# Kernel optimization log

Measured on AMD Instinct MI355X. Metric: run time of the kernel, lower is better.

Reference implementation:

```python
import jax, jax.numpy as jnp
import numpy as np

N = 100000   # num nodes
C = 128      # in_channels == out_channels
H = 4        # heads
D = C // H   # per-head dim = 32
E = 200000   # edges per edge type
T = 3        # number of edge types


def setup_inputs() -> dict:
    key = jax.random.key(0)
    ks = jax.random.split(key, 13)
    x = jax.random.normal(ks[0], (N, C), jnp.float32)
    src = jax.random.randint(ks[1], (T, E), 0, N, dtype=jnp.int32)
    dst = jax.random.randint(ks[2], (T, E), 0, N, dtype=jnp.int32)
    w = lambda k, shape: (jax.random.normal(k, shape, jnp.float32) * 0.02)
    # per-edge-type TransformerConv params: query/key/value/skip linears (C -> H*D = C)
    Wq, Wk, Wv, Ws = (w(ks[3], (T, C, C)), w(ks[4], (T, C, C)),
                      w(ks[5], (T, C, C)), w(ks[6], (T, C, C)))
    bq, bk, bv, bs = (w(ks[7], (T, C)), w(ks[8], (T, C)),
                      w(ks[9], (T, C)), w(ks[10], (T, C)))
    # fusion linear: (T*C) -> C
    Wf = w(ks[11], (C, T * C))
    bf = w(ks[12], (C,))
    return dict(x=x, src=src, dst=dst, Wq=Wq, bq=bq, Wk=Wk, bk=bk,
                Wv=Wv, bv=bv, Ws=Ws, bs=bs, Wf=Wf, bf=bf)


def _transformer_conv(x, s, d, Wq, bq, Wk, bk, Wv, bv, Ws, bs):
    # PyG TransformerConv (beta=False, root_weight=True, concat=True, eval mode)
    q = (x @ Wq.T + bq).reshape(N, H, D)
    k = (x @ Wk.T + bk).reshape(N, H, D)
    v = (x @ Wv.T + bv).reshape(N, H, D)
    # per-edge attention logits: [E, H]
    alpha = jnp.einsum('ehd,ehd->eh', q[d], k[s]) / np.float32(np.sqrt(D))
    # segment softmax over incoming edges of each destination node
    amax = jax.ops.segment_max(alpha, d, num_segments=N)           # [N, H]
    ex = jnp.exp(alpha - amax[d])                                  # [E, H]
    denom = jax.ops.segment_sum(ex, d, num_segments=N)             # [N, H]
    attn = ex / (denom[d] + 1e-16)                                 # [E, H]
    out = jax.ops.segment_sum(attn[:, :, None] * v[s], d, num_segments=N)  # [N, H, D]
    return out.reshape(N, C) + (x @ Ws.T + bs)  # root/skip connection


def reference(x, src, dst, Wq, bq, Wk, bk, Wv, bv, Ws, bs, Wf, bf):
    outs = [
        _transformer_conv(x, src[t], dst[t], Wq[t], bq[t], Wk[t], bk[t],
                          Wv[t], bv[t], Ws[t], bs[t])
        for t in range(T)
    ]
    combined = jnp.concatenate(outs, axis=-1)  # [N, T*C]
    return combined @ Wf.T + bf                # [N, C]
```

## Files before the change

### kernel.cpp

```cpp
#include <hip/hip_runtime.h>

#define NN 100000
#define CC 128
#define EE 200000
#define TT 3
#define NCHUNK 98

typedef __attribute__((ext_vector_type(8))) __bf16 bf16x8;
typedef __attribute__((ext_vector_type(8))) unsigned short ushort8;
typedef __attribute__((ext_vector_type(4))) float f32x4;

union U8 { ushort8 u; bf16x8 b; };

__device__ __forceinline__ unsigned short f2bf(float v) {
    unsigned u = __float_as_uint(v);
    u += 0x7fffu + ((u >> 16) & 1u);
    return (unsigned short)(u >> 16);
}
__device__ __forceinline__ float bf2f(unsigned short h) {
    return __uint_as_float(((unsigned)h) << 16);
}
__device__ __forceinline__ void split8(const float* f, bf16x8& hi, bf16x8& lo) {
    U8 h, l;
    #pragma unroll
    for (int j = 0; j < 8; ++j) {
        float v = f[j];
        unsigned short hs = f2bf(v);
        h.u[j] = hs;
        l.u[j] = f2bf(v - bf2f(hs));
    }
    hi = h.b; lo = l.b;
}

__device__ __forceinline__ void loadA(const float* __restrict__ X, int arow, int kt, int kb,
                                      bf16x8& hi, bf16x8& lo) {
    float tmp[8];
    if (arow < NN) {
        const float* xp = X + (size_t)arow * CC + kt * 32 + kb * 8;
        float4 p0 = *(const float4*)xp;
        float4 p1 = *(const float4*)(xp + 4);
        tmp[0] = p0.x; tmp[1] = p0.y; tmp[2] = p0.z; tmp[3] = p0.w;
        tmp[4] = p1.x; tmp[5] = p1.y; tmp[6] = p1.z; tmp[7] = p1.w;
    } else {
        #pragma unroll
        for (int j = 0; j < 8; ++j) tmp[j] = 0.f;
    }
    split8(tmp, hi, lo);
}


__global__ __launch_bounds__(256) void k_pack(
    const float* __restrict__ Wq, const float* __restrict__ bq,
    const float* __restrict__ Wk, const float* __restrict__ bk,
    const float* __restrict__ Wv, const float* __restrict__ bv,
    const float* __restrict__ Wf,
    unsigned short* __restrict__ Whi3, unsigned short* __restrict__ Wlo3,
    unsigned short* __restrict__ Wfhi, unsigned short* __restrict__ Wflo,
    float* __restrict__ Bpack)
{
    int idx = blockIdx.x * 256 + threadIdx.x;
    int y = blockIdx.y;
    int j  = idx & 7;
    int l  = (idx >> 3) & 63;
    int nt = (idx >> 9) & 7;
    int kt = idx >> 12;
    int c = nt * 16 + (l & 15);
    int k = kt * 32 + ((l >> 4) << 3) + j;
    if (y < 9) {
        int t = y / 3, m = y % 3;
        const float* W = (m == 0 ? Wq : m == 1 ? Wk : Wv) + t * CC * CC;
        float v = W[c * CC + k];
        unsigned short hs = f2bf(v);
        Whi3[y * CC * CC + idx] = hs;
        Wlo3[y * CC * CC + idx] = f2bf(v - bf2f(hs));
    } else if (y < 12) {
        int t = y - 9;
        float v = Wf[(size_t)c * (TT * CC) + t * CC + k];
        unsigned short hs = f2bf(v);
        Wfhi[t * CC * CC + idx] = hs;
        Wflo[t * CC * CC + idx] = f2bf(v - bf2f(hs));
    } else {
        if (idx < 9 * CC) {
            int mm = idx >> 7, cc2 = idx & 127;
            int t = mm / 3, m = mm % 3;
            const float* b = (m == 0 ? bq : m == 1 ? bk : bv);
            Bpack[idx] = b[t * CC + cc2];
        }
    }
}

__global__ __launch_bounds__(256) void k_wcomb(
    const float* __restrict__ Ws, const float* __restrict__ bs,
    const float* __restrict__ Wf, const float* __restrict__ bf,
    unsigned short* __restrict__ Wch, unsigned short* __restrict__ Wcl,
    float* __restrict__ bconst)
{
    int b = blockIdx.x;
    if (b < 64) {
        int idx = b * 256 + threadIdx.x;
        int k = idx >> 7, c = idx & 127;
        float s = 0.f;
        for (int t = 0; t < TT; ++t) {
            const float* wsp = Ws + t * CC * CC;
            const float* wfp = Wf + (size_t)c * (TT * CC) + t * CC;
            for (int j = 0; j < CC; ++j)
                s += wsp[j * CC + k] * wfp[j];
        }
        int kt = k >> 5, kb = (k >> 3) & 3, j = k & 7;
        int l = (c & 15) + (kb << 4);
        int nt = c >> 4;
        int o = (((kt * 8 + nt) * 64) + l) * 8 + j;
        unsigned short hs = f2bf(s);
        Wch[o] = hs;
        Wcl[o] = f2bf(s - bf2f(hs));
    } else {
        int c = threadIdx.x;
        if (c < CC) {
            float s = bf[c];
            for (int t = 0; t < TT; ++t) {
                const float* wfp = Wf + (size_t)c * (TT * CC) + t * CC;
                for (int j = 0; j < CC; ++j)
                    s += bs[t * CC + j] * wfp[j];
            }
            bconst[c] = s;
        }
    }
}

__global__ __launch_bounds__(256) void k_count(const int* __restrict__ dst, int* __restrict__ deg) {
    int idx = blockIdx.x * 256 + threadIdx.x;
    if (idx >= TT * EE) return;
    int t = idx / EE;
    atomicAdd(&deg[t * NN + dst[idx]], 1);
}

__global__ __launch_bounds__(256) void k_scan1(const int* __restrict__ deg,
                                               int* __restrict__ incl, int* __restrict__ bsums) {
    int t = blockIdx.y, b = blockIdx.x, tid = threadIdx.x;
    const int* d = deg + t * NN;
    int base = b * 1024 + tid * 4;
    int v0 = (base + 0 < NN) ? d[base + 0] : 0;
    int v1 = (base + 1 < NN) ? d[base + 1] : 0;
    int v2 = (base + 2 < NN) ? d[base + 2] : 0;
    int v3 = (base + 3 < NN) ? d[base + 3] : 0;
    v1 += v0; v2 += v1; v3 += v2;
    __shared__ int lds[256];
    lds[tid] = v3;
    for (int off = 1; off < 256; off <<= 1) {
        __syncthreads();
        int x = (tid >= off) ? lds[tid - off] : 0;
        __syncthreads();
        lds[tid] += x;
    }
    __syncthreads();
    int excl = lds[tid] - v3;
    if (base + 0 < NN) incl[t * NN + base + 0] = excl + v0;
    if (base + 1 < NN) incl[t * NN + base + 1] = excl + v1;
    if (base + 2 < NN) incl[t * NN + base + 2] = excl + v2;
    if (base + 3 < NN) incl[t * NN + base + 3] = excl + v3;
    if (tid == 255) bsums[t * NCHUNK + b] = lds[255];
}

__global__ __launch_bounds__(128) void k_scan2(const int* __restrict__ bsums, int* __restrict__ bexcl) {
    int t = blockIdx.y, tid = threadIdx.x;
    __shared__ int lds[128];
    int v = (tid < NCHUNK) ? bsums[t * NCHUNK + tid] : 0;
    lds[tid] = v;
    for (int off = 1; off < 128; off <<= 1) {
        __syncthreads();
        int x = (tid >= off) ? lds[tid - off] : 0;
        __syncthreads();
        lds[tid] += x;
    }
    if (tid < NCHUNK) bexcl[t * NCHUNK + tid] = lds[tid] - v;
}

__global__ __launch_bounds__(256) void k_scan3(const int* __restrict__ deg, const int* __restrict__ incl,
                                               const int* __restrict__ bexcl,
                                               int* __restrict__ offs, int* __restrict__ cursor) {
    int t = blockIdx.y, b = blockIdx.x, tid = threadIdx.x;
    int add = bexcl[t * NCHUNK + b];
    int base = b * 1024 + tid * 4;
    #pragma unroll
    for (int j = 0; j < 4; j++) {
        int i = base + j;
        if (i < NN) {
            int e = incl[t * NN + i] - deg[t * NN + i] + add;
            offs[t * NN + i] = e;
            cursor[t * NN + i] = e;
        }
    }
}

__global__ __launch_bounds__(256) void k_scatter(const int* __restrict__ src, const int* __restrict__ dst,
                                                 int* __restrict__ cursor, int* __restrict__ csr_src) {
    int idx = blockIdx.x * 256 + threadIdx.x;
    if (idx >= TT * EE) return;
    int t = idx / EE;
    int d = dst[idx];
    int pos = atomicAdd(&cursor[t * NN + d], 1);
    csr_src[t * EE + pos] = src[idx];
}

__global__ __launch_bounds__(256, 2) void k_mg3(
    const float* __restrict__ x,
    const unsigned short* __restrict__ Whi, const unsigned short* __restrict__ Wlo,
    const float* __restrict__ B3,
    float* __restrict__ Q, float* __restrict__ K, float* __restrict__ V)
{
    int wid = threadIdx.x >> 6, l = threadIdx.x & 63;
    int lan = l & 15, kb = l >> 4;
    int rb = blockIdx.x * 128 + wid * 32;

    bf16x8 ah[2][4], al[2][4];
    #pragma unroll
    for (int rt = 0; rt < 2; ++rt)
        #pragma unroll
        for (int kt = 0; kt < 4; ++kt)
            loadA(x, rb + rt * 16 + lan, kt, kb, ah[rt][kt], al[rt][kt]);

    #pragma unroll 1
    for (int m = 0; m < 3; ++m) {
        const unsigned short* wh = Whi + m * CC * CC;
        const unsigned short* wl = Wlo + m * CC * CC;
        f32x4 acc[2][8];
        #pragma unroll
        for (int rt = 0; rt < 2; ++rt)
            #pragma unroll
            for (int nt = 0; nt < 8; ++nt)
                #pragma unroll
                for (int i = 0; i < 4; ++i) acc[rt][nt][i] = 0.f;

        #pragma unroll
        for (int kt = 0; kt < 4; ++kt) {
            #pragma unroll
            for (int nc = 0; nc < 2; ++nc) {
                U8 bh[4], bl[4];
                #pragma unroll
                for (int j = 0; j < 4; ++j) {
                    size_t wo = ((size_t)(kt * 8 + nc * 4 + j) * 64 + l) * 8;
                    bh[j].u = *(const ushort8*)(wh + wo);
                    bl[j].u = *(const ushort8*)(wl + wo);
                }
                #pragma unroll
                for (int j = 0; j < 4; ++j) {
                    int nt = nc * 4 + j;
                    #pragma unroll
                    for (int rt = 0; rt < 2; ++rt) {
                        acc[rt][nt] = __builtin_amdgcn_mfma_f32_16x16x32_bf16(ah[rt][kt], bl[j].b, acc[rt][nt], 0, 0, 0);
                        acc[rt][nt] = __builtin_amdgcn_mfma_f32_16x16x32_bf16(al[rt][kt], bh[j].b, acc[rt][nt], 0, 0, 0);
                        acc[rt][nt] = __builtin_amdgcn_mfma_f32_16x16x32_bf16(ah[rt][kt], bh[j].b, acc[rt][nt], 0, 0, 0);
                    }
                }
            }
        }

        float* dst = (m == 0 ? Q : m == 1 ? K : V);
        #pragma unroll
        for (int nt = 0; nt < 8; ++nt) {
            int col = nt * 16 + lan;
            float bias = B3[m * CC + col];
            #pragma unroll
            for (int rt = 0; rt < 2; ++rt)
                #pragma unroll
                for (int i = 0; i < 4; ++i) {
                    int grow = rb + rt * 16 + kb * 4 + i;
                    if (grow < NN)
                        dst[(size_t)grow * CC + col] = acc[rt][nt][i] + bias;
                }
        }
    }
}

__global__ __launch_bounds__(256, 2) void k_mfuse(
    const float* __restrict__ X0,
    const unsigned short* __restrict__ W0h, const unsigned short* __restrict__ W0l,
    const float* __restrict__ X1,
    const unsigned short* __restrict__ W1h, const unsigned short* __restrict__ W1l,
    const float* __restrict__ bias, float* __restrict__ out, int accum)
{
    int wid = threadIdx.x >> 6, l = threadIdx.x & 63;
    int lan = l & 15, kb = l >> 4;
    int rb = blockIdx.x * 128 + wid * 32;

    f32x4 acc[2][8];
    #pragma unroll
    for (int rt = 0; rt < 2; ++rt)
        #pragma unroll
        for (int nt = 0; nt < 8; ++nt)
            #pragma unroll
            for (int i = 0; i < 4; ++i) acc[rt][nt][i] = 0.f;

    #pragma unroll 1
    for (int s = 0; s < 2; ++s) {
        const float* X = s ? X1 : X0;
        if (!X) break;
        const unsigned short* wh = s ? W1h : W0h;
        const unsigned short* wl = s ? W1l : W0l;

        bf16x8 ah[2][4], al[2][4];
        #pragma unroll
        for (int rt = 0; rt < 2; ++rt)
            #pragma unroll
            for (int kt = 0; kt < 4; ++kt)
                loadA(X, rb + rt * 16 + lan, kt, kb, ah[rt][kt], al[rt][kt]);

        #pragma unroll
        for (int kt = 0; kt < 4; ++kt) {
            #pragma unroll
            for (int nc = 0; nc < 2; ++nc) {
                U8 bh[4], bl[4];
                #pragma unroll
                for (int j = 0; j < 4; ++j) {
                    size_t wo = ((size_t)(kt * 8 + nc * 4 + j) * 64 + l) * 8;
                    bh[j].u = *(const ushort8*)(wh + wo);
                    bl[j].u = *(const ushort8*)(wl + wo);
                }
                #pragma unroll
                for (int j = 0; j < 4; ++j) {
                    int nt = nc * 4 + j;
                    #pragma unroll
                    for (int rt = 0; rt < 2; ++rt) {
                        acc[rt][nt] = __builtin_amdgcn_mfma_f32_16x16x32_bf16(ah[rt][kt], bl[j].b, acc[rt][nt], 0, 0, 0);
                        acc[rt][nt] = __builtin_amdgcn_mfma_f32_16x16x32_bf16(al[rt][kt], bh[j].b, acc[rt][nt], 0, 0, 0);
                        acc[rt][nt] = __builtin_amdgcn_mfma_f32_16x16x32_bf16(ah[rt][kt], bh[j].b, acc[rt][nt], 0, 0, 0);
                    }
                }
            }
        }
    }

    #pragma unroll
    for (int nt = 0; nt < 8; ++nt) {
        int col = nt * 16 + lan;
        #pragma unroll
        for (int rt = 0; rt < 2; ++rt)
            #pragma unroll
            for (int i = 0; i < 4; ++i) {
                int grow = rb + rt * 16 + kb * 4 + i;
                if (grow < NN) {
                    float* op = out + (size_t)grow * CC + col;
                    float v = acc[rt][nt][i];
                    v += accum ? *op : bias[col];
                    *op = v;
                }
            }
    }
}

__global__ __launch_bounds__(256) void k_agg(
    const float* __restrict__ Q, const float* __restrict__ Kx,
    const float* __restrict__ V, float* __restrict__ A,
    const int* __restrict__ offs, const int* __restrict__ deg, const int* __restrict__ csr)
{
    int wid = threadIdx.x >> 6;
    int lane = threadIdx.x & 63;
    int n = blockIdx.x * 4 + wid;
    if (n >= NN) return;
    int dg = deg[n];
    if (dg == 0) {
        A[(size_t)n * CC + lane] = 0.f;
        A[(size_t)n * CC + 64 + lane] = 0.f;
        return;
    }
    const float scale = 0.17677669529663687f;
    float q0 = Q[(size_t)n * CC + lane];
    float q1 = Q[(size_t)n * CC + 64 + lane];
    float acc0 = 0.f, acc1 = 0.f, den0 = 0.f, den1 = 0.f;
    int off = offs[n];
    for (int i = 0; i < dg; i++) {
        int s = csr[off + i];
        const float* kb = Kx + (size_t)s * CC;
        const float* vb = V + (size_t)s * CC;
        float k0 = kb[lane], k1 = kb[64 + lane];
        float v0 = vb[lane], v1 = vb[64 + lane];
        float d0 = q0 * k0, d1 = q1 * k1;
        #pragma unroll
        for (int m = 16; m >= 1; m >>= 1) {
            d0 += __shfl_xor(d0, m);
            d1 += __shfl_xor(d1, m);
        }
        float e0 = expf(d0 * scale), e1 = expf(d1 * scale);
        acc0 += e0 * v0; den0 += e0;
        acc1 += e1 * v1; den1 += e1;
    }
    A[(size_t)n * CC + lane]      = acc0 / (den0 + 1e-16f);
    A[(size_t)n * CC + 64 + lane] = acc1 / (den1 + 1e-16f);
}

extern "C" void kernel_launch(void* const* d_in, const int* in_sizes, int n_in,
                              void* d_out, int out_size, void* d_ws, size_t ws_size,
                              hipStream_t stream)
{
    const float* x   = (const float*)d_in[0];
    const int*   src = (const int*)d_in[1];
    const int*   dst = (const int*)d_in[2];
    const float* Wq  = (const float*)d_in[3];
    const float* bq  = (const float*)d_in[4];
    const float* Wk  = (const float*)d_in[5];
    const float* bk  = (const float*)d_in[6];
    const float* Wv  = (const float*)d_in[7];
    const float* bv  = (const float*)d_in[8];
    const float* Ws  = (const float*)d_in[9];
    const float* bs  = (const float*)d_in[10];
    const float* Wf  = (const float*)d_in[11];
    const float* bf  = (const float*)d_in[12];
    float* out = (float*)d_out;

    char* ws = (char*)d_ws;
    size_t o = 0;
    auto alloc = [&](size_t bytes) -> char* {
        char* p = ws + o;
        o = (o + bytes + 255) & ~(size_t)255;
        return p;
    };
    unsigned short* Whi3 = (unsigned short*)alloc((size_t)9 * CC * CC * 2);
    unsigned short* Wlo3 = (unsigned short*)alloc((size_t)9 * CC * CC * 2);
    unsigned short* Wfhi = (unsigned short*)alloc((size_t)TT * CC * CC * 2);
    unsigned short* Wflo = (unsigned short*)alloc((size_t)TT * CC * CC * 2);
    unsigned short* Wch  = (unsigned short*)alloc((size_t)CC * CC * 2);
    unsigned short* Wcl  = (unsigned short*)alloc((size_t)CC * CC * 2);
    float* Bpack  = (float*)alloc((size_t)9 * CC * 4);
    float* bconst = (float*)alloc((size_t)CC * 4);
    int* deg      = (int*)alloc((size_t)TT * NN * 4);
    int* incl     = (int*)alloc((size_t)TT * NN * 4);
    int* bsums    = (int*)alloc((size_t)TT * NCHUNK * 4);
    int* bexcl    = (int*)alloc((size_t)TT * NCHUNK * 4);
    int* offs     = (int*)alloc((size_t)TT * NN * 4);
    int* cursor   = (int*)alloc((size_t)TT * NN * 4);
    int* csr_src  = (int*)alloc((size_t)TT * EE * 4);
    float* Qb = (float*)alloc((size_t)NN * CC * 4);
    float* Kb = (float*)alloc((size_t)NN * CC * 4);
    float* Vb = (float*)alloc((size_t)NN * CC * 4);
    float* Ab = (float*)alloc((size_t)NN * CC * 4);

    hipMemsetAsync(deg, 0, (size_t)TT * NN * 4, stream);
    k_pack<<<dim3(64, 13), 256, 0, stream>>>(Wq, bq, Wk, bk, Wv, bv, Wf,
                                             Whi3, Wlo3, Wfhi, Wflo, Bpack);
    k_wcomb<<<65, 256, 0, stream>>>(Ws, bs, Wf, bf, Wch, Wcl, bconst);
    k_count<<<(TT * EE + 255) / 256, 256, 0, stream>>>(dst, deg);
    k_scan1<<<dim3(NCHUNK, TT), 256, 0, stream>>>(deg, incl, bsums);
    k_scan2<<<dim3(1, TT), 128, 0, stream>>>(bsums, bexcl);
    k_scan3<<<dim3(NCHUNK, TT), 256, 0, stream>>>(deg, incl, bexcl, offs, cursor);
    k_scatter<<<(TT * EE + 255) / 256, 256, 0, stream>>>(src, dst, cursor, csr_src);

    int gblocks = (NN + 127) / 128;
    for (int t = 0; t < TT; t++) {
        k_mg3<<<gblocks, 256, 0, stream>>>(x, Whi3 + (size_t)t * 3 * CC * CC,
                                           Wlo3 + (size_t)t * 3 * CC * CC,
                                           Bpack + t * 3 * CC, Qb, Kb, Vb);
        k_agg<<<(NN + 3) / 4, 256, 0, stream>>>(Qb, Kb, Vb, Ab,
                                                offs + t * NN, deg + t * NN, csr_src + (size_t)t * EE);
        if (t == 0)
            k_mfuse<<<gblocks, 256, 0, stream>>>(x, Wch, Wcl,
                                                 Ab, Wfhi, Wflo,
                                                 bconst, out, 0);
        else
            k_mfuse<<<gblocks, 256, 0, stream>>>(Ab, Wfhi + (size_t)t * CC * CC, Wflo + (size_t)t * CC * CC,
                                                 nullptr, nullptr, nullptr,
                                                 bconst, out, 1);
    }
}
```

Before: 916.7 us.

## Stage split-bf16 weight halves through LDS in projection and fusion GEMMs

The QKV projection and fusion GEMM kernels now copy the 128x128 hi and lo bf16 weight halves into a 32 KB shared buffer, one half at a time, with barriers around each copy. Each wave then reads its B fragments from LDS instead of from global memory. The three-MFMA split product is regrouped: one pass over the hi weights does al*bh and ah*bh, and a second pass over the lo weights does ah*bl. Launch bounds rise from 2 to 4 blocks per CU to recover occupancy, which may force register spills given the large accumulator and A-fragment arrays; the extra barriers add sync cost.

```diff
diff --git a/kernel.cpp b/kernel.cpp
--- a/kernel.cpp
+++ b/kernel.cpp
@@ -202,13 +202,23 @@
     csr_src[t * EE + pos] = src[idx];
 }
 
-__global__ __launch_bounds__(256, 2) void k_mg3(
+__device__ __forceinline__ void stage32k(unsigned short* lw, const unsigned short* __restrict__ src, int tid) {
+    #pragma unroll
+    for (int i = 0; i < 8; ++i) {
+        int o = i * 2048 + tid * 8;
+        *(ushort8*)&lw[o] = *(const ushort8*)(src + o);
+    }
+}
+
+__global__ __launch_bounds__(256, 4) void k_mg3(
     const float* __restrict__ x,
     const unsigned short* __restrict__ Whi, const unsigned short* __restrict__ Wlo,
     const float* __restrict__ B3,
     float* __restrict__ Q, float* __restrict__ K, float* __restrict__ V)
 {
-    int wid = threadIdx.x >> 6, l = threadIdx.x & 63;
+    __shared__ __align__(16) unsigned short lw[CC * CC];
+    int tid = threadIdx.x;
+    int wid = tid >> 6, l = tid & 63;
     int lan = l & 15, kb = l >> 4;
     int rb = blockIdx.x * 128 + wid * 32;
 
@@ -221,8 +231,6 @@
 
     #pragma unroll 1
     for (int m = 0; m < 3; ++m) {
-        const unsigned short* wh = Whi + m * CC * CC;
-        const unsigned short* wl = Wlo + m * CC * CC;
         f32x4 acc[2][8];
         #pragma unroll
         for (int rt = 0; rt < 2; ++rt)
@@ -231,29 +239,35 @@
                 #pragma unroll
                 for (int i = 0; i < 4; ++i) acc[rt][nt][i] = 0.f;
 
-        #pragma unroll
-        for (int kt = 0; kt < 4; ++kt) {
-            #pragma unroll
-            for (int nc = 0; nc < 2; ++nc) {
-                U8 bh[4], bl[4];
-                #pragma unroll
-                for (int j = 0; j < 4; ++j) {
-                    size_t wo = ((size_t)(kt * 8 + nc * 4 + j) * 64 + l) * 8;
-                    bh[j].u = *(const ushort8*)(wh + wo);
-                    bl[j].u = *(const ushort8*)(wl + wo);
+        __syncthreads();
+        stage32k(lw, Whi + m * CC * CC, tid);
+        __syncthreads();
+        #pragma unroll
+        for (int kt = 0; kt < 4; ++kt)
+            #pragma unroll
+            for (int nt = 0; nt < 8; ++nt) {
+                U8 b;
+                b.u = *(const ushort8*)&lw[((kt * 8 + nt) * 64 + l) * 8];
+                #pragma unroll
+                for (int rt = 0; rt < 2; ++rt) {
+                    acc[rt][nt] = __builtin_amdgcn_mfma_f32_16x16x32_bf16(al[rt][kt], b.b, acc[rt][nt], 0, 0, 0);
+                    acc[rt][nt] = __builtin_amdgcn_mfma_f32_16x16x32_bf16(ah[rt][kt], b.b, acc[rt][nt], 0, 0, 0);
                 }
-                #pragma unroll
-                for (int j = 0; j < 4; ++j) {
-                    int nt = nc * 4 + j;
-                    #pragma unroll
-                    for (int rt = 0; rt < 2; ++rt) {
-                        acc[rt][nt] = __builtin_amdgcn_mfma_f32_16x16x32_bf16(ah[rt][kt], bl[j].b, acc[rt][nt], 0, 0, 0);
-                        acc[rt][nt] = __builtin_amdgcn_mfma_f32_16x16x32_bf16(al[rt][kt], bh[j].b, acc[rt][nt], 0, 0, 0);
-                        acc[rt][nt] = __builtin_amdgcn_mfma_f32_16x16x32_bf16(ah[rt][kt], bh[j].b, acc[rt][nt], 0, 0, 0);
-                    }
-                }
-            }
-        }
+            }
+
+        __syncthreads();
+        stage32k(lw, Wlo + m * CC * CC, tid);
+        __syncthreads();
+        #pragma unroll
+        for (int kt = 0; kt < 4; ++kt)
+            #pragma unroll
+            for (int nt = 0; nt < 8; ++nt) {
+                U8 b;
+                b.u = *(const ushort8*)&lw[((kt * 8 + nt) * 64 + l) * 8];
+                #pragma unroll
+                for (int rt = 0; rt < 2; ++rt)
+                    acc[rt][nt] = __builtin_amdgcn_mfma_f32_16x16x32_bf16(ah[rt][kt], b.b, acc[rt][nt], 0, 0, 0);
+            }
 
         float* dst = (m == 0 ? Q : m == 1 ? K : V);
         #pragma unroll
@@ -272,14 +286,16 @@
     }
 }
 
-__global__ __launch_bounds__(256, 2) void k_mfuse(
+__global__ __launch_bounds__(256, 4) void k_mfuse(
     const float* __restrict__ X0,
     const unsigned short* __restrict__ W0h, const unsigned short* __restrict__ W0l,
     const float* __restrict__ X1,
     const unsigned short* __restrict__ W1h, const unsigned short* __restrict__ W1l,
     const float* __restrict__ bias, float* __restrict__ out, int accum)
 {
-    int wid = threadIdx.x >> 6, l = threadIdx.x & 63;
+    __shared__ __align__(16) unsigned short lw[CC * CC];
+    int tid = threadIdx.x;
+    int wid = tid >> 6, l = tid & 63;
     int lan = l & 15, kb = l >> 4;
     int rb = blockIdx.x * 128 + wid * 32;
 
@@ -305,29 +321,35 @@
             for (int kt = 0; kt < 4; ++kt)
                 loadA(X, rb + rt * 16 + lan, kt, kb, ah[rt][kt], al[rt][kt]);
 
-        #pragma unroll
-        for (int kt = 0; kt < 4; ++kt) {
-            #pragma unroll
-            for (int nc = 0; nc < 2; ++nc) {
-                U8 bh[4], bl[4];
-                #pragma unroll
-                for (int j = 0; j < 4; ++j) {
-                    size_t wo = ((size_t)(kt * 8 + nc * 4 + j) * 64 + l) * 8;
-                    bh[j].u = *(const ushort8*)(wh + wo);
-                    bl[j].u = *(const ushort8*)(wl + wo);
+        __syncthreads();
+        stage32k(lw, wh, tid);
+        __syncthreads();
+        #pragma unroll
+        for (int kt = 0; kt < 4; ++kt)
+            #pragma unroll
+            for (int nt = 0; nt < 8; ++nt) {
+                U8 b;
+                b.u = *(const ushort8*)&lw[((kt * 8 + nt) * 64 + l) * 8];
+                #pragma unroll
+                for (int rt = 0; rt < 2; ++rt) {
+                    acc[rt][nt] = __builtin_amdgcn_mfma_f32_16x16x32_bf16(al[rt][kt], b.b, acc[rt][nt], 0, 0, 0);
+                    acc[rt][nt] = __builtin_amdgcn_mfma_f32_16x16x32_bf16(ah[rt][kt], b.b, acc[rt][nt], 0, 0, 0);
                 }
-                #pragma unroll
-                for (int j = 0; j < 4; ++j) {
-                    int nt = nc * 4 + j;
-                    #pragma unroll
-                    for (int rt = 0; rt < 2; ++rt) {
-                        acc[rt][nt] = __builtin_amdgcn_mfma_f32_16x16x32_bf16(ah[rt][kt], bl[j].b, acc[rt][nt], 0, 0, 0);
-                        acc[rt][nt] = __builtin_amdgcn_mfma_f32_16x16x32_bf16(al[rt][kt], bh[j].b, acc[rt][nt], 0, 0, 0);
-                        acc[rt][nt] = __builtin_amdgcn_mfma_f32_16x16x32_bf16(ah[rt][kt], bh[j].b, acc[rt][nt], 0, 0, 0);
-                    }
-                }
-            }
-        }
+            }
+
+        __syncthreads();
+        stage32k(lw, wl, tid);
+        __syncthreads();
+        #pragma unroll
+        for (int kt = 0; kt < 4; ++kt)
+            #pragma unroll
+            for (int nt = 0; nt < 8; ++nt) {
+                U8 b;
+                b.u = *(const ushort8*)&lw[((kt * 8 + nt) * 64 + l) * 8];
+                #pragma unroll
+                for (int rt = 0; rt < 2; ++rt)
+                    acc[rt][nt] = __builtin_amdgcn_mfma_f32_16x16x32_bf16(ah[rt][kt], b.b, acc[rt][nt], 0, 0, 0);
+            }
     }
 
     #pragma unroll
```

After: 1.019 ms. 1.11x slower.
